# Performance work log

Measured on AMD Instinct MI355X. Metric: run time of the kernel, lower is better.

Reference implementation:

```python
import jax, jax.numpy as jnp
import numpy as np

GMIN, GMAX = 0.1, 1.0
DIMS = [3, 256, 256, 256, 1]

def setup_inputs() -> dict:
    key = jax.random.key(0)
    ks = jax.random.split(key, 12)
    inp = {"pos": jax.random.normal(ks[0], (1048576, 3), dtype=jnp.float32)}
    for i in range(4):
        fan_in = DIMS[i]
        bound = 1.0 / np.sqrt(fan_in)
        inp[f"W{i}"] = jax.random.uniform(ks[1 + 2 * i], (fan_in, DIMS[i + 1]), jnp.float32, -bound, bound)
        inp[f"b{i}"] = jax.random.uniform(ks[2 + 2 * i], (DIMS[i + 1],), jnp.float32, -bound, bound)
    for i in range(3):
        inp[f"sigma{i}"] = jax.random.uniform(ks[9 + i], (256,), jnp.float32, GMIN, GMAX)
    return inp

def _gauss(x, sigma):
    # Gaussian activation: exp(-x^2 / (2*sigma^2)), sigma learnable per-feature
    return jnp.exp(-jnp.square(x) / (2.0 * jnp.square(sigma)))

def _softplus8(x):
    # torch Softplus(beta=1, threshold=8): linear beyond threshold
    return jnp.where(x > 8.0, x, jnp.log1p(jnp.exp(jnp.minimum(x, 8.0))))

def reference(pos, W0, b0, W1, b1, W2, b2, W3, b3, sigma0, sigma1, sigma2):
    h = _gauss(pos @ W0 + b0, sigma0)      # [N,256]
    h = _gauss(h @ W1 + b1, sigma1)        # [N,256]
    h = _gauss(h @ W2 + b2, sigma2)        # [N,256]
    return _softplus8(h @ W3 + b3)         # [N,1]
```

## Files before the change

### kernel.cpp

```cpp
#include <hip/hip_runtime.h>
#include <hip/hip_bf16.h>
#include <math.h>

typedef __attribute__((ext_vector_type(8))) short short8;
typedef __attribute__((ext_vector_type(4))) float f32x4;
typedef __attribute__((ext_vector_type(2))) float f32x2;
typedef __attribute__((ext_vector_type(2))) unsigned int uint2v;

#define LOG2E 1.4426950408889634f
#define LN2   0.6931471805599453f

__device__ __forceinline__ unsigned short f2bf(float f) {
    union { float f; unsigned u; } v; v.f = f;
    unsigned u = v.u;
    u += 0x7fffu + ((u >> 16) & 1u);
    return (unsigned short)(u >> 16);
}
__device__ __forceinline__ float bf2f(unsigned short h) {
    union { unsigned u; float f; } v; v.u = ((unsigned)h) << 16;
    return v.f;
}
__device__ __forceinline__ unsigned pk_bf16(float a, float b) {
    __hip_bfloat162 t = __float22bfloat162_rn(float2{a, b});
    union { __hip_bfloat162 b; unsigned u; } v; v.b = t;
    return v.u;
}
__device__ __forceinline__ f32x2 pk_add2(f32x2 a, f32x2 b) {
    f32x2 d;
    asm("v_pk_add_f32 %0, %1, %2" : "=v"(d) : "v"(a), "v"(b));
    return d;
}
__device__ __forceinline__ f32x2 pk_mul2(f32x2 a, f32x2 b) {
    f32x2 d;
    asm("v_pk_mul_f32 %0, %1, %2" : "=v"(d) : "v"(a), "v"(b));
    return d;
}

__global__ void pack_kernel(const float* __restrict__ W0, const float* __restrict__ W1,
                            const float* __restrict__ W2, const float* __restrict__ W3,
                            const float* __restrict__ s0, const float* __restrict__ s1,
                            const float* __restrict__ s2,
                            const float* __restrict__ b0, const float* __restrict__ b1,
                            const float* __restrict__ b2,
                            unsigned short* __restrict__ wp, float* __restrict__ negc) {
    int tid = blockIdx.x * 256 + threadIdx.x;
    if (tid < 8192) {
        int j = tid & 7, lane = (tid >> 3) & 63, ct = (tid >> 9) & 3, w = tid >> 11;
        int k = ((lane >> 4) * 8) + j;
        int n = w * 64 + 4 * (lane & 15) + ct;
        unsigned short v = 0;
        if (k < 9) {
            int d = k / 3, m = k - d * 3;
            float sv = s0[n];
            float sc = sqrtf(LOG2E / (2.0f * sv * sv));
            float wv = W0[d * 256 + n] * sc;
            unsigned short wh = f2bf(wv);
            v = (m == 1) ? f2bf(wv - bf2f(wh)) : wh;
        }
        wp[tid] = v;
    } else if (tid < 139264) {
        int e = tid - 8192;
        const float* W = W1;
        const float* S = s1;
        if (e >= 65536) { W = W2; S = s2; e -= 65536; }
        int j = e & 7, lane = (e >> 3) & 63, ct = (e >> 9) & 3, ks = (e >> 11) & 7, w = e >> 14;
        int k = ks * 32 + ((lane >> 4) * 8) + j;
        int n = w * 64 + 4 * (lane & 15) + ct;
        float sv = S[n];
        float sc = sqrtf(LOG2E / (2.0f * sv * sv));
        wp[tid] = f2bf(W[k * 256 + n] * sc);
    } else if (tid < 143360) {
        int e = tid - 139264;
        int j = e & 7, lane = (e >> 3) & 63, ks = (e >> 9) & 1, w = e >> 10;
        int i16p = lane & 15, qp = lane >> 4;
        int k = w * 64 + ks * 32 + qp * 8 + j;
        float wv = W3[k];
        unsigned short wh = f2bf(wv);
        unsigned short v = 0;
        if (i16p == 0) v = wh;
        else if (i16p == 1) v = f2bf(wv - bf2f(wh));
        wp[139264 + e] = v;
    }
    if (tid < 768) {
        int l = tid >> 8, n = tid & 255;
        const float* s = (l == 0) ? s0 : (l == 1 ? s1 : s2);
        const float* b = (l == 0) ? b0 : (l == 1 ? b1 : b2);
        float sv = s[n], bv = b[n];
        float sc = sqrtf(LOG2E / (2.0f * sv * sv));
        negc[l * 256 + n] = sc * bv;
    }
}

constexpr int ROWS = 64;
constexpr int HSTR = 264;
constexpr int ASTR = 40;

template <int NKS, int SSTR>
__device__ __forceinline__ void layer(const unsigned short* __restrict__ src,
                                      const unsigned short* __restrict__ wpk,
                                      const float* __restrict__ ncp,
                                      unsigned short* __restrict__ hdst,
                                      int w, int i16, int q, bool presync) {
    f32x4 acc[4][4];
#pragma unroll
    for (int rg = 0; rg < 4; ++rg)
#pragma unroll
        for (int ct = 0; ct < 4; ++ct)
            acc[rg][ct] = f32x4{0.f, 0.f, 0.f, 0.f};

    const int lane = q * 16 + i16;
    const short8* wp8 = (const short8*)wpk + (w * NKS * 4) * 64 + lane;
    const unsigned short* abase = src + i16 * SSTR + q * 8;

    __builtin_amdgcn_s_setprio(1);
#pragma unroll
    for (int ks = 0; ks < NKS; ++ks) {
        short8 a[4];
#pragma unroll
        for (int rg = 0; rg < 4; ++rg)
            a[rg] = *(const short8*)(abase + rg * 16 * SSTR + ks * 32);
#pragma unroll
        for (int ct = 0; ct < 4; ++ct) {
            short8 wf = wp8[(ks * 4 + ct) * 64];
#pragma unroll
            for (int rg = 0; rg < 4; ++rg)
                acc[rg][ct] = __builtin_amdgcn_mfma_f32_16x16x32_bf16(a[rg], wf, acc[rg][ct], 0, 0, 0);
        }
    }
    __builtin_amdgcn_s_setprio(0);

    const int ce = w * 64 + 4 * i16;
    const f32x4 T = *(const f32x4*)(ncp + ce);
    f32x2 tb[4];
#pragma unroll
    for (int ct = 0; ct < 4; ++ct) tb[ct] = f32x2{T[ct], T[ct]};
    uint2v av[4][4];
#pragma unroll
    for (int rg = 0; rg < 4; ++rg) {
        float gg[4][4];
#pragma unroll
        for (int ct = 0; ct < 4; ++ct) {
            f32x2 xlo = f32x2{acc[rg][ct][0], acc[rg][ct][1]};
            f32x2 xhi = f32x2{acc[rg][ct][2], acc[rg][ct][3]};
            f32x2 ylo = pk_add2(xlo, tb[ct]);
            f32x2 yhi = pk_add2(xhi, tb[ct]);
            f32x2 wlo = pk_mul2(ylo, ylo);
            f32x2 whi = pk_mul2(yhi, yhi);
            gg[0][ct] = __builtin_amdgcn_exp2f(-wlo[0]);
            gg[1][ct] = __builtin_amdgcn_exp2f(-wlo[1]);
            gg[2][ct] = __builtin_amdgcn_exp2f(-whi[0]);
            gg[3][ct] = __builtin_amdgcn_exp2f(-whi[1]);
        }
#pragma unroll
        for (int rr = 0; rr < 4; ++rr) {
            uint2v v;
            v[0] = pk_bf16(gg[rr][0], gg[rr][1]);
            v[1] = pk_bf16(gg[rr][2], gg[rr][3]);
            av[rg][rr] = v;
        }
    }
    if (presync) __syncthreads();
#pragma unroll
    for (int rg = 0; rg < 4; ++rg) {
        int rbase = rg * 16 + q * 4;
#pragma unroll
        for (int rr = 0; rr < 4; ++rr)
            *(uint2v*)&hdst[(rbase + rr) * HSTR + ce] = av[rg][rr];
    }
    __syncthreads();
}

__global__ __launch_bounds__(256, 4) void mlp_kernel(
    const float* __restrict__ pos,
    const float* __restrict__ b3,
    const unsigned short* __restrict__ Wp,
    const float* __restrict__ negc,
    float* __restrict__ out)
{
    __shared__ unsigned short h[ROWS * HSTR];
    __shared__ unsigned short A0[ROWS * ASTR];

    const int tid  = threadIdx.x;
    const int lane = tid & 63;
    const int wave = tid >> 6;
    const int i16  = lane & 15, q = lane >> 4;
    const long row0 = (long)blockIdx.x * ROWS;

    if (tid < ROWS) {
        const float* pp = pos + (row0 + tid) * 3;
        float p0 = pp[0], p1 = pp[1], p2 = pp[2];
        short h0 = (short)f2bf(p0); short l0 = (short)f2bf(p0 - bf2f((unsigned short)h0));
        short h1 = (short)f2bf(p1); short l1 = (short)f2bf(p1 - bf2f((unsigned short)h1));
        short h2 = (short)f2bf(p2); short l2 = (short)f2bf(p2 - bf2f((unsigned short)h2));
        unsigned short* arow = A0 + tid * ASTR;
        *(short8*)(arow + 0)  = short8{h0, h0, l0, h1, h1, l1, h2, h2};
        *(short8*)(arow + 8)  = short8{l2, 0, 0, 0, 0, 0, 0, 0};
        *(short8*)(arow + 16) = short8{0, 0, 0, 0, 0, 0, 0, 0};
        *(short8*)(arow + 24) = short8{0, 0, 0, 0, 0, 0, 0, 0};
    }
    __syncthreads();

    layer<1, ASTR>(A0, Wp,         negc,        h, wave, i16, q, false);
    layer<8, HSTR>(h,  Wp + 8192,  negc + 256,  h, wave, i16, q, true);
    layer<8, HSTR>(h,  Wp + 73728, negc + 512,  h, wave, i16, q, true);

    {
        const short8* w3p = (const short8*)(Wp + 139264) + (wave * 2) * 64 + lane;
        const unsigned short* ab3 = h + i16 * HSTR + wave * 64 + q * 8;
        f32x4 acc3[4];
#pragma unroll
        for (int rg = 0; rg < 4; ++rg) acc3[rg] = f32x4{0.f, 0.f, 0.f, 0.f};
        __builtin_amdgcn_s_setprio(1);
#pragma unroll
        for (int ks = 0; ks < 2; ++ks) {
            short8 wf = w3p[ks * 64];
#pragma unroll
            for (int rg = 0; rg < 4; ++rg) {
                short8 a = *(const short8*)(ab3 + rg * 16 * HSTR + ks * 32);
                acc3[rg] = __builtin_amdgcn_mfma_f32_16x16x32_bf16(a, wf, acc3[rg], 0, 0, 0);
            }
        }
        __builtin_amdgcn_s_setprio(0);
        float* scr = (float*)A0;
        if (i16 < 2) {
#pragma unroll
            for (int rg = 0; rg < 4; ++rg)
                *(f32x4*)&scr[(wave * 2 + i16) * 64 + rg * 16 + q * 4] = acc3[rg];
        }
        __syncthreads();
        if (tid < 64) {
            float s = 0.f;
#pragma unroll
            for (int g = 0; g < 8; ++g) s += scr[g * 64 + tid];
            float x  = s + b3[0];
            float xm = fminf(x, 8.0f);
            float e  = __builtin_amdgcn_exp2f(xm * LOG2E);
            float sp = __builtin_amdgcn_logf(1.0f + e) * LN2;
            out[row0 + tid] = (x > 8.0f) ? x : sp;
        }
    }
}

extern "C" void kernel_launch(void* const* d_in, const int* in_sizes, int n_in,
                              void* d_out, int out_size, void* d_ws, size_t ws_size,
                              hipStream_t stream) {
    const float* pos = (const float*)d_in[0];
    const float* W0  = (const float*)d_in[1];
    const float* b0  = (const float*)d_in[2];
    const float* W1  = (const float*)d_in[3];
    const float* b1  = (const float*)d_in[4];
    const float* W2  = (const float*)d_in[5];
    const float* b2  = (const float*)d_in[6];
    const float* W3  = (const float*)d_in[7];
    const float* b3  = (const float*)d_in[8];
    const float* s0  = (const float*)d_in[9];
    const float* s1  = (const float*)d_in[10];
    const float* s2  = (const float*)d_in[11];

    unsigned short* wp = (unsigned short*)d_ws;
    float* negc = (float*)((char*)d_ws + 286720);

    pack_kernel<<<560, 256, 0, stream>>>(W0, W1, W2, W3, s0, s1, s2, b0, b1, b2, wp, negc);

    int nrows = in_sizes[0] / 3;
    int nblk  = nrows / ROWS;
    mlp_kernel<<<nblk, 256, 0, stream>>>(pos, b3, wp, negc,
                                         (float*)d_out);
}
```

Baseline: 373.0 us.

## Ping-pong two wave groups so MFMA of one overlaps activation of other

Each block now holds 128 rows and 512 threads, split into two 4-wave groups with separate LDS activation buffers. The groups run staggered, so while one group does the matrix multiplies for a layer the other applies the Gaussian activation and stores to LDS. This hides the exp/convert/store phase behind tensor-core work. The cost is more LDS per block, a barrier after every half-stage, and a launch_bounds of 512 with 4 blocks, which limits registers per thread and may lower occupancy or cause spills.

```diff
diff --git a/kernel.cpp b/kernel.cpp
--- a/kernel.cpp
+++ b/kernel.cpp
@@ -91,27 +91,19 @@
     }
 }
 
-constexpr int ROWS = 64;
 constexpr int HSTR = 264;
 constexpr int ASTR = 40;
 
 template <int NKS, int SSTR>
-__device__ __forceinline__ void layer(const unsigned short* __restrict__ src,
-                                      const unsigned short* __restrict__ wpk,
-                                      const float* __restrict__ ncp,
-                                      unsigned short* __restrict__ hdst,
-                                      int w, int i16, int q, bool presync) {
-    f32x4 acc[4][4];
+__device__ __forceinline__ void mfma_l(const unsigned short* __restrict__ src,
+                                       const short8* __restrict__ wp8,
+                                       f32x4 (&acc)[4][4], int i16, int q) {
 #pragma unroll
     for (int rg = 0; rg < 4; ++rg)
 #pragma unroll
         for (int ct = 0; ct < 4; ++ct)
             acc[rg][ct] = f32x4{0.f, 0.f, 0.f, 0.f};
-
-    const int lane = q * 16 + i16;
-    const short8* wp8 = (const short8*)wpk + (w * NKS * 4) * 64 + lane;
     const unsigned short* abase = src + i16 * SSTR + q * 8;
-
     __builtin_amdgcn_s_setprio(1);
 #pragma unroll
     for (int ks = 0; ks < NKS; ++ks) {
@@ -128,13 +120,16 @@
         }
     }
     __builtin_amdgcn_s_setprio(0);
-
-    const int ce = w * 64 + 4 * i16;
+}
+
+__device__ __forceinline__ void act_store4(f32x4 (&acc)[4][4],
+                                           const float* __restrict__ ncp,
+                                           unsigned short* __restrict__ hdst,
+                                           int ce, int q) {
     const f32x4 T = *(const f32x4*)(ncp + ce);
     f32x2 tb[4];
 #pragma unroll
     for (int ct = 0; ct < 4; ++ct) tb[ct] = f32x2{T[ct], T[ct]};
-    uint2v av[4][4];
 #pragma unroll
     for (int rg = 0; rg < 4; ++rg) {
         float gg[4][4];
@@ -156,37 +151,50 @@
             uint2v v;
             v[0] = pk_bf16(gg[rr][0], gg[rr][1]);
             v[1] = pk_bf16(gg[rr][2], gg[rr][3]);
-            av[rg][rr] = v;
-        }
-    }
-    if (presync) __syncthreads();
-#pragma unroll
-    for (int rg = 0; rg < 4; ++rg) {
-        int rbase = rg * 16 + q * 4;
-#pragma unroll
-        for (int rr = 0; rr < 4; ++rr)
-            *(uint2v*)&hdst[(rbase + rr) * HSTR + ce] = av[rg][rr];
-    }
-    __syncthreads();
-}
-
-__global__ __launch_bounds__(256, 4) void mlp_kernel(
+            *(uint2v*)&hdst[(rg * 16 + q * 4 + rr) * HSTR + ce] = v;
+        }
+    }
+}
+
+__device__ __forceinline__ void l3_mfma(const unsigned short* __restrict__ ab3,
+                                        const short8* __restrict__ w3p,
+                                        f32x4 (&acc3)[4]) {
+#pragma unroll
+    for (int rg = 0; rg < 4; ++rg) acc3[rg] = f32x4{0.f, 0.f, 0.f, 0.f};
+    __builtin_amdgcn_s_setprio(1);
+#pragma unroll
+    for (int ks = 0; ks < 2; ++ks) {
+        short8 wf = w3p[ks * 64];
+#pragma unroll
+        for (int rg = 0; rg < 4; ++rg) {
+            short8 a = *(const short8*)(ab3 + rg * 16 * HSTR + ks * 32);
+            acc3[rg] = __builtin_amdgcn_mfma_f32_16x16x32_bf16(a, wf, acc3[rg], 0, 0, 0);
+        }
+    }
+    __builtin_amdgcn_s_setprio(0);
+}
+
+__global__ __launch_bounds__(512, 4) void mlp_kernel(
     const float* __restrict__ pos,
     const float* __restrict__ b3,
     const unsigned short* __restrict__ Wp,
     const float* __restrict__ negc,
     float* __restrict__ out)
 {
-    __shared__ unsigned short h[ROWS * HSTR];
-    __shared__ unsigned short A0[ROWS * ASTR];
+    __shared__ unsigned short hA[64 * HSTR];
+    __shared__ unsigned short hB[64 * HSTR];
+    __shared__ unsigned short A0[128 * ASTR];
 
     const int tid  = threadIdx.x;
     const int lane = tid & 63;
     const int wave = tid >> 6;
+    const int w4   = wave & 3;
+    const int grp  = wave >> 2;
     const int i16  = lane & 15, q = lane >> 4;
-    const long row0 = (long)blockIdx.x * ROWS;
-
-    if (tid < ROWS) {
+    const int ce   = w4 * 64 + 4 * i16;
+    const long row0 = (long)blockIdx.x * 128;
+
+    if (tid < 128) {
         const float* pp = pos + (row0 + tid) * 3;
         float p0 = pp[0], p1 = pp[1], p2 = pp[2];
         short h0 = (short)f2bf(p0); short l0 = (short)f2bf(p0 - bf2f((unsigned short)h0));
@@ -200,44 +208,73 @@
     }
     __syncthreads();
 
-    layer<1, ASTR>(A0, Wp,         negc,        h, wave, i16, q, false);
-    layer<8, HSTR>(h,  Wp + 8192,  negc + 256,  h, wave, i16, q, true);
-    layer<8, HSTR>(h,  Wp + 73728, negc + 512,  h, wave, i16, q, true);
-
-    {
-        const short8* w3p = (const short8*)(Wp + 139264) + (wave * 2) * 64 + lane;
-        const unsigned short* ab3 = h + i16 * HSTR + wave * 64 + q * 8;
-        f32x4 acc3[4];
-#pragma unroll
-        for (int rg = 0; rg < 4; ++rg) acc3[rg] = f32x4{0.f, 0.f, 0.f, 0.f};
-        __builtin_amdgcn_s_setprio(1);
-#pragma unroll
-        for (int ks = 0; ks < 2; ++ks) {
-            short8 wf = w3p[ks * 64];
-#pragma unroll
-            for (int rg = 0; rg < 4; ++rg) {
-                short8 a = *(const short8*)(ab3 + rg * 16 * HSTR + ks * 32);
-                acc3[rg] = __builtin_amdgcn_mfma_f32_16x16x32_bf16(a, wf, acc3[rg], 0, 0, 0);
-            }
-        }
-        __builtin_amdgcn_s_setprio(0);
-        float* scr = (float*)A0;
+    f32x4 acc[4][4];
+    const short8* wp0 = (const short8*)Wp            + (w4 * 4)  * 64 + lane;
+    const short8* wp1 = (const short8*)(Wp + 8192)   + (w4 * 32) * 64 + lane;
+    const short8* wp2 = (const short8*)(Wp + 73728)  + (w4 * 32) * 64 + lane;
+    const short8* w3p = (const short8*)(Wp + 139264) + (w4 * 2)  * 64 + lane;
+
+    if (!grp) mfma_l<1, ASTR>(A0, wp0, acc, i16, q);
+    __syncthreads();
+    if (!grp) act_store4(acc, negc, hA, ce, q);
+    else      mfma_l<1, ASTR>(A0 + 64 * ASTR, wp0, acc, i16, q);
+    __syncthreads();
+    if (!grp) mfma_l<8, HSTR>(hA, wp1, acc, i16, q);
+    else      act_store4(acc, negc, hB, ce, q);
+    __syncthreads();
+    if (!grp) act_store4(acc, negc + 256, hA, ce, q);
+    else      mfma_l<8, HSTR>(hB, wp1, acc, i16, q);
+    __syncthreads();
+    if (!grp) mfma_l<8, HSTR>(hA, wp2, acc, i16, q);
+    else      act_store4(acc, negc + 256, hB, ce, q);
+    __syncthreads();
+    if (!grp) act_store4(acc, negc + 512, hA, ce, q);
+    else      mfma_l<8, HSTR>(hB, wp2, acc, i16, q);
+    __syncthreads();
+
+    f32x4 acc3[4];
+    float* scrA = (float*)A0;
+    float* scrB = (float*)hA;
+
+    if (!grp) {
+        l3_mfma(hA + i16 * HSTR + w4 * 64 + q * 8, w3p, acc3);
         if (i16 < 2) {
 #pragma unroll
             for (int rg = 0; rg < 4; ++rg)
-                *(f32x4*)&scr[(wave * 2 + i16) * 64 + rg * 16 + q * 4] = acc3[rg];
-        }
-        __syncthreads();
-        if (tid < 64) {
-            float s = 0.f;
-#pragma unroll
-            for (int g = 0; g < 8; ++g) s += scr[g * 64 + tid];
-            float x  = s + b3[0];
-            float xm = fminf(x, 8.0f);
-            float e  = __builtin_amdgcn_exp2f(xm * LOG2E);
-            float sp = __builtin_amdgcn_logf(1.0f + e) * LN2;
-            out[row0 + tid] = (x > 8.0f) ? x : sp;
-        }
+                *(f32x4*)&scrA[(w4 * 2 + i16) * 64 + rg * 16 + q * 4] = acc3[rg];
+        }
+    } else {
+        act_store4(acc, negc + 512, hB, ce, q);
+    }
+    __syncthreads();
+    if (grp) {
+        l3_mfma(hB + i16 * HSTR + w4 * 64 + q * 8, w3p, acc3);
+        if (i16 < 2) {
+#pragma unroll
+            for (int rg = 0; rg < 4; ++rg)
+                *(f32x4*)&scrB[(w4 * 2 + i16) * 64 + rg * 16 + q * 4] = acc3[rg];
+        }
+    } else if (tid < 64) {
+        float s = 0.f;
+#pragma unroll
+        for (int g = 0; g < 8; ++g) s += scrA[g * 64 + tid];
+        float x  = s + b3[0];
+        float xm = fminf(x, 8.0f);
+        float e  = __builtin_amdgcn_exp2f(xm * LOG2E);
+        float sp = __builtin_amdgcn_logf(1.0f + e) * LN2;
+        out[row0 + tid] = (x > 8.0f) ? x : sp;
+    }
+    __syncthreads();
+    if (tid >= 256 && tid < 320) {
+        int r = tid & 63;
+        float s = 0.f;
+#pragma unroll
+        for (int g = 0; g < 8; ++g) s += scrB[g * 64 + r];
+        float x  = s + b3[0];
+        float xm = fminf(x, 8.0f);
+        float e  = __builtin_amdgcn_exp2f(xm * LOG2E);
+        float sp = __builtin_amdgcn_logf(1.0f + e) * LN2;
+        out[row0 + 64 + r] = (x > 8.0f) ? x : sp;
     }
 }
 
@@ -263,7 +300,7 @@
     pack_kernel<<<560, 256, 0, stream>>>(W0, W1, W2, W3, s0, s1, s2, b0, b1, b2, wp, negc);
 
     int nrows = in_sizes[0] / 3;
-    int nblk  = nrows / ROWS;
-    mlp_kernel<<<nblk, 256, 0, stream>>>(pos, b3, wp, negc,
+    int nblk  = nrows / 128;
+    mlp_kernel<<<nblk, 512, 0, stream>>>(pos, b3, wp, negc,
                                          (float*)d_out);
 }
```

After: 393.9 us. 1.06x slower.
